# Kernel optimization log

Measured on AMD Instinct MI355X. Metric: run time of the kernel, lower is better.

## Reference

```python
import jax, jax.numpy as jnp
import numpy as np

N_NODES = 100000
N_EDGES = 1600000
IN_CH = 128
EDGE_CH = 16
OUT_CH = 64
H1, F1 = 8, 8          # gat1: heads=8, out=8, concat -> 64
NEG_SLOPE = 0.2


def _add_self_loops(edge_index, n):
    sl = jnp.arange(n, dtype=edge_index.dtype)
    return jnp.concatenate([edge_index, jnp.stack([sl, sl])], axis=1)


def gat_layer(x, edge_index, W, a_src, a_dst, b, heads, out_dim, concat):
    """PyG-style GATConv (eval mode, self-loops already included in edge_index)."""
    n = x.shape[0]
    src, dst = edge_index[0], edge_index[1]
    xW = (x @ W).reshape(n, heads, out_dim)          # [N,H,F]
    al_src = (xW * a_src).sum(-1)                    # [N,H]
    al_dst = (xW * a_dst).sum(-1)                    # [N,H]
    e = jax.nn.leaky_relu(al_src[src] + al_dst[dst], NEG_SLOPE)  # [E,H]
    # segment softmax over incoming edges of each dst node
    m = jnp.full((n, heads), -jnp.inf, e.dtype).at[dst].max(e)
    w = jnp.exp(e - m[dst])
    denom = jax.ops.segment_sum(w, dst, num_segments=n)
    alpha = w / (denom[dst] + 1e-16)                 # [E,H]
    out = jax.ops.segment_sum(xW[src] * alpha[..., None], dst, num_segments=n)
    out = out.reshape(n, heads * out_dim) if concat else out.mean(axis=1)
    return out + b


def setup_inputs() -> dict:
    key = jax.random.key(0)
    ks = jax.random.split(key, 16)
    p = lambda k, shp: (jax.random.normal(k, shp, jnp.float32) * 0.1)
    inp = {
        "x": jax.random.normal(ks[0], (N_NODES, IN_CH), jnp.float32),
        "edge_index": jax.random.randint(ks[1], (2, N_EDGES), 0, N_NODES, jnp.int64 if jax.config.jax_enable_x64 else jnp.int32),
        "edge_attr": jax.random.normal(ks[2], (N_EDGES, EDGE_CH), jnp.float32),
        "W1": p(ks[3], (IN_CH, H1 * F1)),
        "a_src1": p(ks[4], (H1, F1)),
        "a_dst1": p(ks[5], (H1, F1)),
        "b1": jnp.zeros((H1 * F1,), jnp.float32),
        "W2": p(ks[6], (H1 * F1, OUT_CH)),
        "a_src2": p(ks[7], (1, OUT_CH)),
        "a_dst2": p(ks[8], (1, OUT_CH)),
        "b2": jnp.zeros((OUT_CH,), jnp.float32),
        "lin_W": p(ks[9], (OUT_CH, OUT_CH)),
        "lin_b": jnp.zeros((OUT_CH,), jnp.float32),
        "mlp_W1": p(ks[10], (2 * OUT_CH + EDGE_CH, 128)),
        "mlp_b1": jnp.zeros((128,), jnp.float32),
        "mlp_W2": p(ks[11], (128, 2)),
        "mlp_b2": jnp.zeros((2,), jnp.float32),
    }
    return inp


def reference(x, edge_index, edge_attr, W1, a_src1, a_dst1, b1, W2, a_src2, a_dst2, b2,
              lin_W, lin_b, mlp_W1, mlp_b1, mlp_W2, mlp_b2):
    n = x.shape[0]
    ei_sl = _add_self_loops(edge_index, n)
    h = gat_layer(x, ei_sl, W1, a_src1, a_dst1, b1, H1, F1, concat=True)
    h = jax.nn.elu(h)
    h = gat_layer(h, ei_sl, W2, a_src2, a_dst2, b2, 1, OUT_CH, concat=False)
    h = jax.nn.elu(h)
    h = h @ lin_W + lin_b                              # [N, out]
    src, dst = edge_index[0], edge_index[1]
    ef = jnp.concatenate([h[src], h[dst], edge_attr], axis=1)  # [E, 2*out+edge_ch]
    eo = jax.nn.relu(ef @ mlp_W1 + mlp_b1) @ mlp_W2 + mlp_b2   # [E, 2]
    return jax.nn.log_softmax(eo, axis=1)
```

## Files before the change

### kernel.cpp

```cpp
#include <hip/hip_runtime.h>
#include <math.h>

#define DEV_INLINE __device__ __forceinline__
typedef unsigned short ushort;
typedef __attribute__((ext_vector_type(8))) short bf16x8;
typedef __attribute__((ext_vector_type(4))) float f32x4;

DEV_INLINE float lrelu(float x){ return x > 0.f ? x : 0.2f*x; }
DEV_INLINE float eluf(float x){ return x>0.f? x : (__expf(x)-1.f); }
DEV_INLINE ushort f2bf(float f){
  unsigned u = __float_as_uint(f);
  return (ushort)((u + 0x7FFFu + ((u>>16)&1u)) >> 16);
}
DEV_INLINE float b2f(ushort u){ return __uint_as_float(((unsigned)u)<<16); }

__global__ __launch_bounds__(256) void gemm_n64(const float* __restrict__ A, const float* __restrict__ W,
    const float* __restrict__ bias, ushort* __restrict__ Cb, int n, int K,
    int mode, const float* __restrict__ asrc, const float* __restrict__ adst,
    float* __restrict__ alS, float* __restrict__ alD)
{
  int j = threadIdx.x & 63;
  int node = blockIdx.x*4 + (threadIdx.x>>6);
  if (node >= n) return;
  const float4* A4 = (const float4*)(A + (size_t)node*K);
  float acc = 0.f;
  int K4 = K>>2;
  for (int k4 = 0; k4 < K4; ++k4) {
    float4 a = A4[k4];
    const float* w = W + k4*256 + j;
    acc = fmaf(a.x, w[0],   acc);
    acc = fmaf(a.y, w[64],  acc);
    acc = fmaf(a.z, w[128], acc);
    acc = fmaf(a.w, w[192], acc);
  }
  if (bias) acc += bias[j];
  Cb[(size_t)node*64 + j] = f2bf(acc);
  if (mode == 1) {
    float s = acc * asrc[j];
    float d = acc * adst[j];
    #pragma unroll
    for (int off = 1; off < 8; off <<= 1) { s += __shfl_xor(s, off, 64); d += __shfl_xor(d, off, 64); }
    if ((j & 7) == 0) {
      alS[(size_t)node*8 + (j>>3)] = s;
      alD[(size_t)node*8 + (j>>3)] = d;
    }
  } else if (mode == 2) {
    float s = acc * asrc[j];
    float d = acc * adst[j];
    #pragma unroll
    for (int off = 1; off < 64; off <<= 1) { s += __shfl_xor(s, off, 64); d += __shfl_xor(d, off, 64); }
    if (j == 0) { alS[node] = s; alD[node] = d; }
  }
}

__global__ __launch_bounds__(256) void hist_kernel(const int* __restrict__ dst, int* __restrict__ deg, int E)
{
  int e = blockIdx.x*blockDim.x + threadIdx.x;
  if (e < E) atomicAdd(deg + dst[e], 1);
}

__global__ __launch_bounds__(256) void scan_p1(const int* __restrict__ deg, int* __restrict__ part, int n)
{
  __shared__ int red[256];
  int base = blockIdx.x*1024;
  int s = 0;
  for (int k = threadIdx.x; k < 1024; k += 256) { int i = base+k; s += (i<n)? deg[i] : 0; }
  red[threadIdx.x] = s; __syncthreads();
  for (int off = 128; off > 0; off >>= 1) {
    if (threadIdx.x < off) red[threadIdx.x] += red[threadIdx.x+off];
    __syncthreads();
  }
  if (threadIdx.x == 0) part[blockIdx.x] = red[0];
}

__global__ void scan_p2(int* part, int* rowptr, int nb, int n)
{
  if (threadIdx.x == 0 && blockIdx.x == 0) {
    int run = 0;
    for (int b = 0; b < nb; ++b) { int v = part[b]; part[b] = run; run += v; }
    rowptr[n] = run;
  }
}

__global__ __launch_bounds__(256) void scan_p3(const int* __restrict__ deg, const int* __restrict__ part,
    int* __restrict__ rowptr, int* __restrict__ cursor, int n)
{
  __shared__ int ts[256];
  int tid = threadIdx.x;
  int base = blockIdx.x*1024 + tid*4;
  int v0=0,v1=0,v2=0,v3=0;
  if (base+0 < n) v0 = deg[base+0];
  if (base+1 < n) v1 = deg[base+1];
  if (base+2 < n) v2 = deg[base+2];
  if (base+3 < n) v3 = deg[base+3];
  ts[tid] = v0+v1+v2+v3; __syncthreads();
  for (int off = 1; off < 256; off <<= 1) {
    int t = (tid >= off) ? ts[tid-off] : 0;
    __syncthreads();
    ts[tid] += t;
    __syncthreads();
  }
  int ex = part[blockIdx.x] + (tid ? ts[tid-1] : 0);
  if (base+0 < n) { rowptr[base+0] = ex; cursor[base+0] = ex; ex += v0; }
  if (base+1 < n) { rowptr[base+1] = ex; cursor[base+1] = ex; ex += v1; }
  if (base+2 < n) { rowptr[base+2] = ex; cursor[base+2] = ex; ex += v2; }
  if (base+3 < n) { rowptr[base+3] = ex; cursor[base+3] = ex; ex += v3; }
}

__global__ __launch_bounds__(256) void scatter_kernel(const int* __restrict__ src, const int* __restrict__ dst,
    int* __restrict__ cursor, int* __restrict__ csr, int E)
{
  int e = blockIdx.x*blockDim.x + threadIdx.x;
  if (e >= E) return;
  int pos = atomicAdd(cursor + dst[e], 1);
  csr[pos] = src[e];
}

__global__ __launch_bounds__(256) void agg1(const ushort* __restrict__ xWb, const float* __restrict__ alS,
    const float* __restrict__ alD, const int* __restrict__ rowptr, const int* __restrict__ csr,
    const float* __restrict__ b, float* __restrict__ outp, int n)
{
  int node = blockIdx.x*4 + (threadIdx.x>>6);
  if (node >= n) return;
  int l = threadIdx.x & 63, h = l >> 3;
  float aD  = alD[(size_t)node*8 + h];
  float m   = lrelu(alS[(size_t)node*8 + h] + aD);
  float den = 1.f;
  float acc = b2f(xWb[(size_t)node*64 + l]);
  int p = rowptr[node], p1 = rowptr[node+1];
  for (; p+1 < p1; p += 2) {
    int s0 = csr[p], s1 = csr[p+1];
    float e0 = lrelu(alS[(size_t)s0*8 + h] + aD);
    float e1 = lrelu(alS[(size_t)s1*8 + h] + aD);
    float x0 = b2f(xWb[(size_t)s0*64 + l]);
    float x1 = b2f(xWb[(size_t)s1*64 + l]);
    float mn = fmaxf(m, fmaxf(e0, e1));
    float sc = __expf(m - mn);
    float w0 = __expf(e0 - mn);
    float w1 = __expf(e1 - mn);
    den = den*sc + w0 + w1;
    acc = acc*sc + w0*x0 + w1*x1;
    m = mn;
  }
  if (p < p1) {
    int s0 = csr[p];
    float e0 = lrelu(alS[(size_t)s0*8 + h] + aD);
    float x0 = b2f(xWb[(size_t)s0*64 + l]);
    float mn = fmaxf(m, e0);
    float sc = __expf(m - mn);
    float w0 = __expf(e0 - mn);
    den = den*sc + w0;
    acc = acc*sc + w0*x0;
    m = mn;
  }
  outp[(size_t)node*64 + l] = eluf(acc/(den + 1e-16f) + b[l]);
}

__global__ __launch_bounds__(256) void agg2(const ushort* __restrict__ xWb, const float* __restrict__ alS,
    const float* __restrict__ alD, const int* __restrict__ rowptr, const int* __restrict__ csr,
    const float* __restrict__ b, float* __restrict__ outp, int n)
{
  int node = blockIdx.x*4 + (threadIdx.x>>6);
  if (node >= n) return;
  int l = threadIdx.x & 63;
  float aD  = alD[node];
  float m   = lrelu(alS[node] + aD);
  float den = 1.f;
  float acc = b2f(xWb[(size_t)node*64 + l]);
  int p = rowptr[node], p1 = rowptr[node+1];
  for (; p+1 < p1; p += 2) {
    int s0 = csr[p], s1 = csr[p+1];
    float e0 = lrelu(alS[s0] + aD);
    float e1 = lrelu(alS[s1] + aD);
    float x0 = b2f(xWb[(size_t)s0*64 + l]);
    float x1 = b2f(xWb[(size_t)s1*64 + l]);
    float mn = fmaxf(m, fmaxf(e0, e1));
    float sc = __expf(m - mn);
    float w0 = __expf(e0 - mn);
    float w1 = __expf(e1 - mn);
    den = den*sc + w0 + w1;
    acc = acc*sc + w0*x0 + w1*x1;
    m = mn;
  }
  if (p < p1) {
    int s0 = csr[p];
    float e0 = lrelu(alS[s0] + aD);
    float x0 = b2f(xWb[(size_t)s0*64 + l]);
    float mn = fmaxf(m, e0);
    float sc = __expf(m - mn);
    float w0 = __expf(e0 - mn);
    den = den*sc + w0;
    acc = acc*sc + w0*x0;
    m = mn;
  }
  outp[(size_t)node*64 + l] = eluf(acc/(den + 1e-16f) + b[l]);
}

__global__ void w1_swizzle(const float* __restrict__ W1, ushort* __restrict__ w1sw)
{
  int t = blockIdx.x*blockDim.x + threadIdx.x;
  if (t >= 2560) return;
  int l = t & 63, nk = t >> 6;
  int nt = nk/5, ks = nk - nt*5;
  int ncol = nt*16 + (l&15);
  int kb = ks*32 + (l>>4)*8;
  union { ushort u[8]; uint4 q; } v;
  #pragma unroll
  for (int j = 0; j < 8; ++j) {
    int k = kb + j;
    float f = (k < 144) ? W1[k*128 + ncol] : 0.f;
    v.u[j] = f2bf(f);
  }
  ((uint4*)w1sw)[t] = v.q;
}

__global__ __launch_bounds__(256) void edge_mlp_mfma(
    const ushort* __restrict__ h3b, const float* __restrict__ attr,
    const int* __restrict__ src, const int* __restrict__ dst,
    const ushort* __restrict__ w1sw, const float* __restrict__ b1,
    const float* __restrict__ W2, const float* __restrict__ b2,
    float* __restrict__ out, int E)
{
  __shared__ uint4 W1s[2560];
  for (int i = threadIdx.x; i < 2560; i += 256) W1s[i] = ((const uint4*)w1sw)[i];
  __syncthreads();
  const bf16x8* Bf = (const bf16x8*)W1s;

  const int lane = threadIdx.x & 63;
  const int quad = lane >> 4, l15 = lane & 15;

  float w2a[8], w2b[8], bia[8];
  #pragma unroll
  for (int nt = 0; nt < 8; ++nt) {
    w2a[nt] = W2[(nt*16 + l15)*2 + 0];
    w2b[nt] = W2[(nt*16 + l15)*2 + 1];
    bia[nt] = b1[nt*16 + l15];
  }
  const float bb0 = b2[0], bb1 = b2[1];

  const int wid = (blockIdx.x*256 + threadIdx.x) >> 6;
  const int nw  = gridDim.x*4;
  const int nT  = (E + 15) >> 4;

  for (int t = wid; t < nT; t += nw) {
    const int tb = t*16;
    int e = tb + l15; if (e >= E) e = E - 1;
    const int s = src[e], d = dst[e];

    bf16x8 a0 = *(const bf16x8*)(h3b + (size_t)s*64 + quad*8);
    bf16x8 a1 = *(const bf16x8*)(h3b + (size_t)s*64 + 32 + quad*8);
    bf16x8 a2 = *(const bf16x8*)(h3b + (size_t)d*64 + quad*8);
    bf16x8 a3 = *(const bf16x8*)(h3b + (size_t)d*64 + 32 + quad*8);
    bf16x8 a4 = {};
    if (quad < 2) {
      const float4* ap = (const float4*)(attr + (size_t)e*16 + quad*8);
      float4 f0 = ap[0], f1 = ap[1];
      a4[0] = (short)f2bf(f0.x); a4[1] = (short)f2bf(f0.y);
      a4[2] = (short)f2bf(f0.z); a4[3] = (short)f2bf(f0.w);
      a4[4] = (short)f2bf(f1.x); a4[5] = (short)f2bf(f1.y);
      a4[6] = (short)f2bf(f1.z); a4[7] = (short)f2bf(f1.w);
    }

    f32x4 acc[8];
    #pragma unroll
    for (int nt = 0; nt < 8; ++nt) acc[nt] = (f32x4){0.f,0.f,0.f,0.f};

    #pragma unroll
    for (int nt = 0; nt < 8; ++nt) {
      acc[nt] = __builtin_amdgcn_mfma_f32_16x16x32_bf16(a0, Bf[(nt*5+0)*64 + lane], acc[nt], 0,0,0);
      acc[nt] = __builtin_amdgcn_mfma_f32_16x16x32_bf16(a1, Bf[(nt*5+1)*64 + lane], acc[nt], 0,0,0);
      acc[nt] = __builtin_amdgcn_mfma_f32_16x16x32_bf16(a2, Bf[(nt*5+2)*64 + lane], acc[nt], 0,0,0);
      acc[nt] = __builtin_amdgcn_mfma_f32_16x16x32_bf16(a3, Bf[(nt*5+3)*64 + lane], acc[nt], 0,0,0);
      acc[nt] = __builtin_amdgcn_mfma_f32_16x16x32_bf16(a4, Bf[(nt*5+4)*64 + lane], acc[nt], 0,0,0);
    }

    #pragma unroll
    for (int r = 0; r < 4; ++r) {
      float p0 = 0.f, p1 = 0.f;
      #pragma unroll
      for (int nt = 0; nt < 8; ++nt) {
        float hv = fmaxf(acc[nt][r] + bia[nt], 0.f);
        p0 = fmaf(hv, w2a[nt], p0);
        p1 = fmaf(hv, w2b[nt], p1);
      }
      #pragma unroll
      for (int off = 1; off < 16; off <<= 1) {
        p0 += __shfl_xor(p0, off, 64);
        p1 += __shfl_xor(p1, off, 64);
      }
      if (l15 == 0) {
        int eo = tb + quad*4 + r;
        if (eo < E) {
          p0 += bb0; p1 += bb1;
          float mm = fmaxf(p0, p1);
          float ls = mm + __logf(__expf(p0-mm) + __expf(p1-mm));
          ((float2*)out)[eo] = make_float2(p0 - ls, p1 - ls);
        }
      }
    }
  }
}

extern "C" void kernel_launch(void* const* d_in, const int* in_sizes, int n_in,
                              void* d_out, int out_size, void* d_ws, size_t ws_size,
                              hipStream_t stream) {
  const float* x      = (const float*)d_in[0];
  const int*   ei     = (const int*)d_in[1];
  const float* attr   = (const float*)d_in[2];
  const float* W1     = (const float*)d_in[3];
  const float* a_src1 = (const float*)d_in[4];
  const float* a_dst1 = (const float*)d_in[5];
  const float* b1     = (const float*)d_in[6];
  const float* W2     = (const float*)d_in[7];
  const float* a_src2 = (const float*)d_in[8];
  const float* a_dst2 = (const float*)d_in[9];
  const float* b2     = (const float*)d_in[10];
  const float* linW   = (const float*)d_in[11];
  const float* linb   = (const float*)d_in[12];
  const float* mW1    = (const float*)d_in[13];
  const float* mb1    = (const float*)d_in[14];
  const float* mW2    = (const float*)d_in[15];
  const float* mb2    = (const float*)d_in[16];
  float* out = (float*)d_out;

  int N = in_sizes[0] / 128;
  int E = in_sizes[1] / 2;
  const int* src = ei;
  const int* dst = ei + E;

  char* ws = (char*)d_ws;
  float*    bufH   = (float*)(ws);
  ushort*   bufAb  = (ushort*)(ws + 25600000);
  ushort*   h3b    = (ushort*)(ws + 38400000);
  int*      csr    = (int*)  (ws + 51200000);
  float*    alS    = (float*)(ws + 57600000);
  float*    alD    = (float*)(ws + 60800000);
  int*      rowptr = (int*)  (ws + 64000000);
  int*      degcur = (int*)  (ws + 64400064);
  int*      part   = (int*)  (ws + 64800064);
  ushort*   w1sw   = (ushort*)(ws + 64900096);

  int gN4 = (N + 3) / 4;
  int gE  = (E + 255) / 256;
  int nChunk = (N + 1023) / 1024;

  hipMemsetAsync(degcur, 0, (size_t)N*sizeof(int), stream);
  hist_kernel<<<gE, 256, 0, stream>>>(dst, degcur, E);
  scan_p1<<<nChunk, 256, 0, stream>>>(degcur, part, N);
  scan_p2<<<1, 64, 0, stream>>>(part, rowptr, nChunk, N);
  scan_p3<<<nChunk, 256, 0, stream>>>(degcur, part, rowptr, degcur, N);
  scatter_kernel<<<gE, 256, 0, stream>>>(src, dst, degcur, csr, E);
  w1_swizzle<<<10, 256, 0, stream>>>(mW1, w1sw);

  gemm_n64<<<gN4, 256, 0, stream>>>(x, W1, nullptr, bufAb, N, 128, 1, a_src1, a_dst1, alS, alD);
  agg1<<<gN4, 256, 0, stream>>>(bufAb, alS, alD, rowptr, csr, b1, bufH, N);
  gemm_n64<<<gN4, 256, 0, stream>>>(bufH, W2, nullptr, bufAb, N, 64, 2, a_src2, a_dst2, alS, alD);
  agg2<<<gN4, 256, 0, stream>>>(bufAb, alS, alD, rowptr, csr, b2, bufH, N);
  gemm_n64<<<gN4, 256, 0, stream>>>(bufH, linW, linb, h3b, N, 64, 0, nullptr, nullptr, nullptr, nullptr);
  edge_mlp_mfma<<<1024, 256, 0, stream>>>(h3b, attr, src, dst, w1sw, mb1, mW2, mb2, out, E);
}
```

Before: 1.214 ms.

## Parallelize block-sum scan, unroll aggregation by four, double edge-MLP grid

The single-thread serial prefix over chunk partials becomes a 128-thread shared-memory Hillis-Steele scan. The GAT aggregation loops in agg1 and agg2 handle four neighbors per online-softmax step instead of two, which gives more gathers in flight and fewer rescale exponentials. The edge MLP launch grid goes from 1024 to 2048 blocks. The new scan assumes at most 128 chunks (N up to 131072), which holds here with 98 chunks.

```diff
diff --git a/kernel.cpp b/kernel.cpp
--- a/kernel.cpp
+++ b/kernel.cpp
@@ -73,13 +73,21 @@
   if (threadIdx.x == 0) part[blockIdx.x] = red[0];
 }
 
-__global__ void scan_p2(int* part, int* rowptr, int nb, int n)
-{
-  if (threadIdx.x == 0 && blockIdx.x == 0) {
-    int run = 0;
-    for (int b = 0; b < nb; ++b) { int v = part[b]; part[b] = run; run += v; }
-    rowptr[n] = run;
-  }
+__global__ __launch_bounds__(128) void scan_p2(int* part, int* rowptr, int nb, int n)
+{
+  __shared__ int ts[128];
+  int tid = threadIdx.x;
+  int v = (tid < nb) ? part[tid] : 0;
+  ts[tid] = v; __syncthreads();
+  #pragma unroll
+  for (int off = 1; off < 128; off <<= 1) {
+    int t = (tid >= off) ? ts[tid-off] : 0;
+    __syncthreads();
+    ts[tid] += t;
+    __syncthreads();
+  }
+  if (tid < nb) part[tid] = ts[tid] - v;
+  if (tid == 127) rowptr[n] = ts[127];
 }
 
 __global__ __launch_bounds__(256) void scan_p3(const int* __restrict__ deg, const int* __restrict__ part,
@@ -128,21 +136,25 @@
   float den = 1.f;
   float acc = b2f(xWb[(size_t)node*64 + l]);
   int p = rowptr[node], p1 = rowptr[node+1];
-  for (; p+1 < p1; p += 2) {
-    int s0 = csr[p], s1 = csr[p+1];
+  for (; p+3 < p1; p += 4) {
+    int s0 = csr[p], s1 = csr[p+1], s2 = csr[p+2], s3 = csr[p+3];
     float e0 = lrelu(alS[(size_t)s0*8 + h] + aD);
     float e1 = lrelu(alS[(size_t)s1*8 + h] + aD);
+    float e2 = lrelu(alS[(size_t)s2*8 + h] + aD);
+    float e3 = lrelu(alS[(size_t)s3*8 + h] + aD);
     float x0 = b2f(xWb[(size_t)s0*64 + l]);
     float x1 = b2f(xWb[(size_t)s1*64 + l]);
-    float mn = fmaxf(m, fmaxf(e0, e1));
+    float x2 = b2f(xWb[(size_t)s2*64 + l]);
+    float x3 = b2f(xWb[(size_t)s3*64 + l]);
+    float mn = fmaxf(fmaxf(m, fmaxf(e0, e1)), fmaxf(e2, e3));
     float sc = __expf(m - mn);
-    float w0 = __expf(e0 - mn);
-    float w1 = __expf(e1 - mn);
-    den = den*sc + w0 + w1;
-    acc = acc*sc + w0*x0 + w1*x1;
+    float w0 = __expf(e0 - mn), w1 = __expf(e1 - mn);
+    float w2 = __expf(e2 - mn), w3 = __expf(e3 - mn);
+    den = den*sc + (w0 + w1) + (w2 + w3);
+    acc = acc*sc + (w0*x0 + w1*x1) + (w2*x2 + w3*x3);
     m = mn;
   }
-  if (p < p1) {
+  for (; p < p1; ++p) {
     int s0 = csr[p];
     float e0 = lrelu(alS[(size_t)s0*8 + h] + aD);
     float x0 = b2f(xWb[(size_t)s0*64 + l]);
@@ -168,21 +180,25 @@
   float den = 1.f;
   float acc = b2f(xWb[(size_t)node*64 + l]);
   int p = rowptr[node], p1 = rowptr[node+1];
-  for (; p+1 < p1; p += 2) {
-    int s0 = csr[p], s1 = csr[p+1];
+  for (; p+3 < p1; p += 4) {
+    int s0 = csr[p], s1 = csr[p+1], s2 = csr[p+2], s3 = csr[p+3];
     float e0 = lrelu(alS[s0] + aD);
     float e1 = lrelu(alS[s1] + aD);
+    float e2 = lrelu(alS[s2] + aD);
+    float e3 = lrelu(alS[s3] + aD);
     float x0 = b2f(xWb[(size_t)s0*64 + l]);
     float x1 = b2f(xWb[(size_t)s1*64 + l]);
-    float mn = fmaxf(m, fmaxf(e0, e1));
+    float x2 = b2f(xWb[(size_t)s2*64 + l]);
+    float x3 = b2f(xWb[(size_t)s3*64 + l]);
+    float mn = fmaxf(fmaxf(m, fmaxf(e0, e1)), fmaxf(e2, e3));
     float sc = __expf(m - mn);
-    float w0 = __expf(e0 - mn);
-    float w1 = __expf(e1 - mn);
-    den = den*sc + w0 + w1;
-    acc = acc*sc + w0*x0 + w1*x1;
+    float w0 = __expf(e0 - mn), w1 = __expf(e1 - mn);
+    float w2 = __expf(e2 - mn), w3 = __expf(e3 - mn);
+    den = den*sc + (w0 + w1) + (w2 + w3);
+    acc = acc*sc + (w0*x0 + w1*x1) + (w2*x2 + w3*x3);
     m = mn;
   }
-  if (p < p1) {
+  for (; p < p1; ++p) {
     int s0 = csr[p];
     float e0 = lrelu(alS[s0] + aD);
     float x0 = b2f(xWb[(size_t)s0*64 + l]);
@@ -347,7 +363,7 @@
   hipMemsetAsync(degcur, 0, (size_t)N*sizeof(int), stream);
   hist_kernel<<<gE, 256, 0, stream>>>(dst, degcur, E);
   scan_p1<<<nChunk, 256, 0, stream>>>(degcur, part, N);
-  scan_p2<<<1, 64, 0, stream>>>(part, rowptr, nChunk, N);
+  scan_p2<<<1, 128, 0, stream>>>(part, rowptr, nChunk, N);
   scan_p3<<<nChunk, 256, 0, stream>>>(degcur, part, rowptr, degcur, N);
   scatter_kernel<<<gE, 256, 0, stream>>>(src, dst, degcur, csr, E);
   w1_swizzle<<<10, 256, 0, stream>>>(mW1, w1sw);
@@ -357,5 +373,5 @@
   gemm_n64<<<gN4, 256, 0, stream>>>(bufH, W2, nullptr, bufAb, N, 64, 2, a_src2, a_dst2, alS, alD);
   agg2<<<gN4, 256, 0, stream>>>(bufAb, alS, alD, rowptr, csr, b2, bufH, N);
   gemm_n64<<<gN4, 256, 0, stream>>>(bufH, linW, linb, h3b, N, 64, 0, nullptr, nullptr, nullptr, nullptr);
-  edge_mlp_mfma<<<1024, 256, 0, stream>>>(h3b, attr, src, dst, w1sw, mb1, mW2, mb2, out, E);
-}
+  edge_mlp_mfma<<<2048, 256, 0, stream>>>(h3b, attr, src, dst, w1sw, mb1, mW2, mb2, out, E);
+}
```

Result: faster. 1.153 ms (-5.0%).
